# Performance work log

Hardware: AMD Instinct MI355X
Metric: run time of the kernel (lower is better)

## Reference

```python
import jax, jax.numpy as jnp
import numpy as np

DECAY = 0.6
THRESH = 0.6
MASK_T = 784 * 4  # default T in create_general_mask


def _make_mask(dim, c_min=10, c_max=50, min_dc=0.95, max_dc=0.99, T=MASK_T):
    # Faithful numpy port of create_general_mask (phase_shift_max=0.0 -> no shift).
    dcs = np.linspace(min_dc, max_dc, dim)
    cycles = np.linspace(c_min, c_max, dim)
    rows = []
    for cyc, dc in zip(cycles, dcs):
        cyc = int(np.ceil(cyc))
        on = int(np.ceil(dc * cyc))
        pat = [1] * on + [0] * (cyc - on)
        full = pat * (T // cyc) + pat[: T % cyc]
        rows.append(full)
    return jnp.asarray(np.array(rows, dtype=np.float32))  # [dim, T]


def setup_inputs() -> dict:
    key = jax.random.key(0)
    k1, k2, k3, k4, k5 = jax.random.split(key, 5)
    T, B, NTOKEN, NINP, H1, H2 = 128, 32, 32000, 256, 512, 512
    raw_input = jax.random.randint(k1, (T, B), 0, NTOKEN)
    enc_w = jax.random.uniform(k2, (NTOKEN, NINP), jnp.float32, -0.1, 0.1)
    # kaiming_uniform-like init: bound = sqrt(6 / fan_in), torch fan_in = dim 1
    b1 = float(np.sqrt(6.0 / H1))
    b2 = float(np.sqrt(6.0 / H2))
    fc1 = jax.random.uniform(k3, (NINP, H1), jnp.float32, -b1, b1)
    fc2 = jax.random.uniform(k4, (H1, H2), jnp.float32, -b2, b2)
    dec_w = jax.random.uniform(k5, (NTOKEN, H2), jnp.float32, -0.1, 0.1)
    dec_b = jnp.zeros((NTOKEN,), jnp.float32)
    mask1 = _make_mask(H1)
    mask2 = _make_mask(H2)
    return {"raw_input": raw_input, "enc_w": enc_w, "fc1": fc1, "fc2": fc2,
            "dec_w": dec_w, "dec_b": dec_b, "mask1": mask1, "mask2": mask2}


def _act(x):
    # ActFun.forward: heaviside spike
    return (x > 0.0).astype(x.dtype)


def reference(raw_input, enc_w, fc1, fc2, dec_w, dec_b, mask1, mask2):
    T, B = raw_input.shape
    emb = enc_w[raw_input]                    # [T, B, ninp] (dropout p=0 -> identity)
    m1 = mask1[:, :T].T                       # [T, H1]
    m2 = mask2[:, :T].T                       # [T, H2]

    def rhythm_update(fc, x, mem, m):
        state = x @ fc                        # [B, H]
        reset = (mem > THRESH).astype(x.dtype)
        new_mem = mem * (1.0 - reset) * DECAY + state
        mem = jnp.where(m == 0.0, mem, new_mem)   # mask broadcasts [H] -> [B, H]
        spike = _act(mem - THRESH) * m
        return mem, spike

    h1 = jnp.zeros((B, fc1.shape[1]), emb.dtype)
    h2 = jnp.zeros((B, fc2.shape[1]), emb.dtype)

    def step(carry, xs):
        h1m, h2m = carry
        x, ma, mb = xs
        h1m, s1 = rhythm_update(fc1, x, h1m, ma)
        h2m, s2 = rhythm_update(fc2, s1, h2m, mb)
        return (h1m, h2m), s2

    _, spikes = jax.lax.scan(step, (h1, h2), (emb, m1, m2))  # [T, B, H2]
    decoded = spikes @ dec_w.T + dec_b        # [T, B, ntoken]
    return decoded
```

## Files before the change

### kernel.cpp

```cpp
#include <hip/hip_runtime.h>


typedef __attribute__((ext_vector_type(8))) short short8;
typedef __attribute__((ext_vector_type(4))) float f32x4;
typedef __attribute__((ext_vector_type(8))) unsigned short us8;

__device__ __forceinline__ unsigned short f2bf(float f) {
    unsigned int u = __float_as_uint(f);
    unsigned int r = (u + 0x7FFFu + ((u >> 16) & 1u)) >> 16;
    return (unsigned short)r;
}

__global__ __launch_bounds__(256) void split_kernel(
    const float* __restrict__ w, unsigned short* __restrict__ w2, int n4)
{
    int i = blockIdx.x * 256 + threadIdx.x;
    if (i >= n4) return;
    float4 v = ((const float4*)w)[i];
    float vv[4] = {v.x, v.y, v.z, v.w};
    us8 o;
    #pragma unroll
    for (int c = 0; c < 4; ++c) {
        unsigned short hb = f2bf(vv[c]);
        float hf = __uint_as_float(((unsigned int)hb) << 16);
        o[2 * c]     = hb;
        o[2 * c + 1] = f2bf(vv[c] - hf);
    }
    ((us8*)w2)[i] = o;
}

__global__ __launch_bounds__(256) void gemm_f32_kernel(
    const float* __restrict__ A, const float* __restrict__ B,
    float* __restrict__ C, int M, int N, int K,
    const int* __restrict__ gidx, const float* __restrict__ gtable)
{
    __shared__ float As[16][64];
    __shared__ float Bs[16][64];
    int tid = threadIdx.x;
    int bn0 = blockIdx.x * 64, bm0 = blockIdx.y * 64;

    int lrowA = tid >> 2;
    int lkA   = (tid & 3) * 4;
    int lkB   = tid >> 4;
    int lnB   = (tid & 15) * 4;
    int ty = tid >> 4, tx = tid & 15;

    const float* Abase;
    size_t aoff;
    int grow = bm0 + lrowA;
    if (gidx) { Abase = gtable; aoff = (size_t)gidx[grow] * K; }
    else      { Abase = A;      aoff = (size_t)grow * K; }

    float acc[4][4];
    #pragma unroll
    for (int i = 0; i < 4; ++i)
        #pragma unroll
        for (int j = 0; j < 4; ++j) acc[i][j] = 0.f;

    for (int k0 = 0; k0 < K; k0 += 16) {
        float4 av = *(const float4*)(Abase + aoff + k0 + lkA);
        As[lkA + 0][lrowA] = av.x;
        As[lkA + 1][lrowA] = av.y;
        As[lkA + 2][lrowA] = av.z;
        As[lkA + 3][lrowA] = av.w;
        float4 bv = *(const float4*)(B + (size_t)(k0 + lkB) * N + bn0 + lnB);
        *(float4*)&Bs[lkB][lnB] = bv;
        __syncthreads();
        #pragma unroll
        for (int kk = 0; kk < 16; ++kk) {
            float4 aq = *(float4*)&As[kk][ty * 4];
            float4 bq = *(float4*)&Bs[kk][tx * 4];
            float aa[4] = {aq.x, aq.y, aq.z, aq.w};
            float bb[4] = {bq.x, bq.y, bq.z, bq.w};
            #pragma unroll
            for (int i = 0; i < 4; ++i)
                #pragma unroll
                for (int j = 0; j < 4; ++j) acc[i][j] += aa[i] * bb[j];
        }
        __syncthreads();
    }
    #pragma unroll
    for (int i = 0; i < 4; ++i) {
        float4 v = {acc[i][0], acc[i][1], acc[i][2], acc[i][3]};
        *(float4*)(C + (size_t)(bm0 + ty * 4 + i) * N + bn0 + tx * 4) = v;
    }
}

template <int DUP>
__global__ __launch_bounds__(64) void scan_kernel(
    const float* __restrict__ state, const float* __restrict__ mask,
    float* __restrict__ outF, unsigned int* __restrict__ outU)
{
    int tid = blockIdx.x * 64 + threadIdx.x;
    int b = tid >> 9, h = tid & 511;
    const float* mrow = mask + (size_t)h * 3136;
    float mem = 0.f;
    #pragma unroll
    for (int t = 0; t < 128; ++t) {
        size_t ridx = (size_t)(t * 32 + b) * 512 + h;
        float st = state[ridx];
        float m  = mrow[t];
        float nm = (mem > 0.6f) ? st : mem * 0.6f + st;
        mem = (m == 0.0f) ? mem : nm;
        float spf = (mem > 0.6f) ? m : 0.0f;
        if (DUP) {
            unsigned int bb = f2bf(spf);
            outU[ridx] = bb * 0x10001u;
        } else {
            outF[ridx] = spf;
        }
    }
}

__global__ __launch_bounds__(256) void gemm3_kernel(
    const unsigned short* __restrict__ A,
    const unsigned short* __restrict__ W,
    const float* __restrict__ bias, float* __restrict__ C)
{
    constexpr int K = 1024, NTOK = 32000;
    __shared__ unsigned short sA[128 * 64];
    __shared__ unsigned short sB[128 * 64];

    int tid  = threadIdx.x;
    int lane = tid & 63;
    int wid  = __builtin_amdgcn_readfirstlane(tid >> 6);

    int bid = blockIdx.x;
    int swz = (bid & 7) * 1000 + (bid >> 3);
    int mt = swz & 31;
    int nt = swz >> 5;
    int m0 = mt * 128, n0 = nt * 128;

    int wm = wid >> 1, wn = wid & 1;

    f32x4 acc[4][4];
    #pragma unroll
    for (int i = 0; i < 4; ++i)
        #pragma unroll
        for (int j = 0; j < 4; ++j) acc[i][j] = (f32x4){0.f, 0.f, 0.f, 0.f};

    for (int it = 0; it < 16; ++it) {
        int k0 = it * 64;

        #pragma unroll
        for (int i = 0; i < 4; ++i) {
            int q   = i * 256 + wid * 64 + lane;
            int row = q >> 3;
            int cb  = q & 7;
            int scb = cb ^ (row & 7);
            const unsigned short* ga = A + (size_t)(m0 + row) * K + k0 + scb * 8;
            const unsigned short* gb = W + (size_t)(n0 + row) * K + k0 + scb * 8;
            unsigned short* la = sA + (size_t)(i * 256 + wid * 64) * 8;
            unsigned short* lb = sB + (size_t)(i * 256 + wid * 64) * 8;
            __builtin_amdgcn_global_load_lds(
                (const __attribute__((address_space(1))) unsigned int*)ga,
                (__attribute__((address_space(3))) unsigned int*)la, 16, 0, 0);
            __builtin_amdgcn_global_load_lds(
                (const __attribute__((address_space(1))) unsigned int*)gb,
                (__attribute__((address_space(3))) unsigned int*)lb, 16, 0, 0);
        }
        __syncthreads();

        #pragma unroll
        for (int ks = 0; ks < 2; ++ks) {
            short8 fa[4], fb[4];
            int kb = ks * 64 + ((lane >> 4) << 4);
            #pragma unroll
            for (int f = 0; f < 4; ++f) {
                int rowA = wm * 64 + f * 16 + (lane & 15);
                int adA  = rowA * 128 + (kb ^ ((rowA & 7) << 4));
                fa[f] = *(const short8*)((const char*)sA + adA);
                int rowB = wn * 64 + f * 16 + (lane & 15);
                int adB  = rowB * 128 + (kb ^ ((rowB & 7) << 4));
                fb[f] = *(const short8*)((const char*)sB + adB);
            }
            #pragma unroll
            for (int mf = 0; mf < 4; ++mf)
                #pragma unroll
                for (int nf = 0; nf < 4; ++nf)
                    acc[mf][nf] = __builtin_amdgcn_mfma_f32_16x16x32_bf16(
                        fa[mf], fb[nf], acc[mf][nf], 0, 0, 0);
        }
        __syncthreads();
    }

    int lr = lane >> 4, lc = lane & 15;
    #pragma unroll
    for (int mf = 0; mf < 4; ++mf) {
        #pragma unroll
        for (int nf = 0; nf < 4; ++nf) {
            int gr = m0 + wm * 64 + mf * 16 + lr * 4;
            int gc = n0 + wn * 64 + nf * 16 + lc;
            float bv = bias[gc];
            f32x4 v = acc[mf][nf];
            #pragma unroll
            for (int j = 0; j < 4; ++j)
                C[(size_t)(gr + j) * NTOK + gc] = v[j] + bv;
        }
    }
}

extern "C" void kernel_launch(void* const* d_in, const int* in_sizes, int n_in,
                              void* d_out, int out_size, void* d_ws, size_t ws_size,
                              hipStream_t stream)
{
    const int*   raw   = (const int*)  d_in[0];
    const float* enc_w = (const float*)d_in[1];
    const float* fc1   = (const float*)d_in[2];
    const float* fc2   = (const float*)d_in[3];
    const float* dec_w = (const float*)d_in[4];
    const float* dec_b = (const float*)d_in[5];
    const float* mask1 = (const float*)d_in[6];
    const float* mask2 = (const float*)d_in[7];
    float* out = (float*)d_out;

    const int T = 128, B = 32, H1 = 512, H2 = 512, NINP = 256, NTOK = 32000;
    const int M = T * B;

    char* ws = (char*)d_ws;
    float*          st  = (float*)ws;
    float*          spF = (float*)(ws + (size_t)(8u << 20));
    unsigned int*   a2u = (unsigned int*)(ws + (size_t)(8u << 20));
    unsigned short* A2  = (unsigned short*)(ws + (size_t)(8u << 20));
    unsigned short* W2  = (unsigned short*)(ws + (size_t)(16u << 20));

    int n4 = NTOK * H2 / 4;
    split_kernel<<<(n4 + 255) / 256, 256, 0, stream>>>(dec_w, W2, n4);

    gemm_f32_kernel<<<dim3(H1 / 64, M / 64), 256, 0, stream>>>(
        nullptr, fc1, st, M, H1, NINP, raw, enc_w);

    scan_kernel<0><<<(B * H1) / 64, 64, 0, stream>>>(st, mask1, spF, nullptr);

    gemm_f32_kernel<<<dim3(H2 / 64, M / 64), 256, 0, stream>>>(
        spF, fc2, st, M, H2, H1, nullptr, nullptr);

    scan_kernel<1><<<(B * H2) / 64, 64, 0, stream>>>(st, mask2, nullptr, a2u);

    gemm3_kernel<<<(M / 128) * (NTOK / 128), 256, 0, stream>>>(A2, W2, dec_b, out);

    (void)in_sizes; (void)n_in; (void)out_size; (void)ws_size;
}
```

Before: 931.0 us.

## Rewrite decoder GEMM as 256x256 tile with 4-stage async LDS pipeline

```diff
diff --git a/kernel.cpp b/kernel.cpp
--- a/kernel.cpp
+++ b/kernel.cpp
@@ -4,11 +4,23 @@
 typedef __attribute__((ext_vector_type(8))) short short8;
 typedef __attribute__((ext_vector_type(4))) float f32x4;
 typedef __attribute__((ext_vector_type(8))) unsigned short us8;
+
+#define WAITVM(N) asm volatile("s_waitcnt vmcnt(" #N ")" ::: "memory")
 
 __device__ __forceinline__ unsigned short f2bf(float f) {
     unsigned int u = __float_as_uint(f);
     unsigned int r = (u + 0x7FFFu + ((u >> 16) & 1u)) >> 16;
     return (unsigned short)r;
+}
+
+__global__ __launch_bounds__(256) void maskT_kernel(
+    const float* __restrict__ m1, const float* __restrict__ m2,
+    float* __restrict__ t1, float* __restrict__ t2)
+{
+    int i = blockIdx.x * 256 + threadIdx.x;
+    int h = i >> 7, t = i & 127;
+    t1[t * 512 + h] = m1[(size_t)h * 3136 + t];
+    t2[t * 512 + h] = m2[(size_t)h * 3136 + t];
 }
 
 __global__ __launch_bounds__(256) void split_kernel(
@@ -88,110 +100,138 @@
 
 template <int DUP>
 __global__ __launch_bounds__(64) void scan_kernel(
-    const float* __restrict__ state, const float* __restrict__ mask,
+    const float* __restrict__ state, const float* __restrict__ maskT,
     float* __restrict__ outF, unsigned int* __restrict__ outU)
 {
     int tid = blockIdx.x * 64 + threadIdx.x;
     int b = tid >> 9, h = tid & 511;
-    const float* mrow = mask + (size_t)h * 3136;
     float mem = 0.f;
-    #pragma unroll
+    #pragma unroll 8
     for (int t = 0; t < 128; ++t) {
         size_t ridx = (size_t)(t * 32 + b) * 512 + h;
         float st = state[ridx];
-        float m  = mrow[t];
+        float m  = maskT[t * 512 + h];
         float nm = (mem > 0.6f) ? st : mem * 0.6f + st;
         mem = (m == 0.0f) ? mem : nm;
         float spf = (mem > 0.6f) ? m : 0.0f;
-        if (DUP) {
-            unsigned int bb = f2bf(spf);
-            outU[ridx] = bb * 0x10001u;
-        } else {
-            outF[ridx] = spf;
-        }
-    }
-}
-
-__global__ __launch_bounds__(256) void gemm3_kernel(
+        if (DUP) outU[ridx] = f2bf(spf) * 0x10001u;
+        else     outF[ridx] = spf;
+    }
+}
+
+__global__ __launch_bounds__(512, 2) void gemm3_kernel(
     const unsigned short* __restrict__ A,
     const unsigned short* __restrict__ W,
     const float* __restrict__ bias, float* __restrict__ C)
 {
     constexpr int K = 1024, NTOK = 32000;
-    __shared__ unsigned short sA[128 * 64];
-    __shared__ unsigned short sB[128 * 64];
+    __shared__ char lds[131072];
 
     int tid  = threadIdx.x;
     int lane = tid & 63;
     int wid  = __builtin_amdgcn_readfirstlane(tid >> 6);
 
     int bid = blockIdx.x;
-    int swz = (bid & 7) * 1000 + (bid >> 3);
-    int mt = swz & 31;
-    int nt = swz >> 5;
-    int m0 = mt * 128, n0 = nt * 128;
-
-    int wm = wid >> 1, wn = wid & 1;
-
-    f32x4 acc[4][4];
-    #pragma unroll
-    for (int i = 0; i < 4; ++i)
+    int swz = (bid & 7) * 250 + (bid >> 3);
+    int mt = swz & 15;
+    int nt = swz >> 4;
+    int m0 = mt * 256, n0 = nt * 256;
+
+    int wm = wid >> 2, wn = wid & 3;
+
+    const unsigned short* srcB[4];
+    int dstOff[4];
+    #pragma unroll
+    for (int i = 0; i < 4; ++i) {
+        int q   = i * 512 + tid;
+        int isB = q >> 10;
+        int qq  = q & 1023;
+        int row = qq >> 2;
+        int cp  = qq & 3;
+        int c   = cp ^ ((row + (row >> 2)) & 3);
+        srcB[i] = (isB ? W + (size_t)(n0 + row) * K
+                       : A + (size_t)(m0 + row) * K) + c * 8;
+        dstOff[i] = (i * 512 + wid * 64) * 16;
+    }
+
+    int r = lane & 15, co = lane >> 4;
+    int aOff[8], bOff[4];
+    #pragma unroll
+    for (int mf = 0; mf < 8; ++mf) {
+        int row = wm * 128 + mf * 16 + r;
+        aOff[mf] = row * 64 + ((co ^ ((row + (row >> 2)) & 3)) * 16);
+    }
+    #pragma unroll
+    for (int nf = 0; nf < 4; ++nf) {
+        int row = wn * 64 + nf * 16 + r;
+        bOff[nf] = 16384 + row * 64 + ((co ^ ((row + (row >> 2)) & 3)) * 16);
+    }
+
+    f32x4 acc[8][4];
+    #pragma unroll
+    for (int i = 0; i < 8; ++i)
         #pragma unroll
         for (int j = 0; j < 4; ++j) acc[i][j] = (f32x4){0.f, 0.f, 0.f, 0.f};
 
-    for (int it = 0; it < 16; ++it) {
-        int k0 = it * 64;
-
+    auto STAGE = [&](int slot, int kt) {
         #pragma unroll
         for (int i = 0; i < 4; ++i) {
-            int q   = i * 256 + wid * 64 + lane;
-            int row = q >> 3;
-            int cb  = q & 7;
-            int scb = cb ^ (row & 7);
-            const unsigned short* ga = A + (size_t)(m0 + row) * K + k0 + scb * 8;
-            const unsigned short* gb = W + (size_t)(n0 + row) * K + k0 + scb * 8;
-            unsigned short* la = sA + (size_t)(i * 256 + wid * 64) * 8;
-            unsigned short* lb = sB + (size_t)(i * 256 + wid * 64) * 8;
             __builtin_amdgcn_global_load_lds(
-                (const __attribute__((address_space(1))) unsigned int*)ga,
-                (__attribute__((address_space(3))) unsigned int*)la, 16, 0, 0);
-            __builtin_amdgcn_global_load_lds(
-                (const __attribute__((address_space(1))) unsigned int*)gb,
-                (__attribute__((address_space(3))) unsigned int*)lb, 16, 0, 0);
+                (const __attribute__((address_space(1))) unsigned int*)(srcB[i] + kt * 32),
+                (__attribute__((address_space(3))) unsigned int*)(lds + (slot << 15) + dstOff[i]),
+                16, 0, 0);
         }
-        __syncthreads();
-
-        #pragma unroll
-        for (int ks = 0; ks < 2; ++ks) {
-            short8 fa[4], fb[4];
-            int kb = ks * 64 + ((lane >> 4) << 4);
+    };
+    auto COMPUTE = [&](int t) {
+        const char* base = lds + ((t & 3) << 15);
+        short8 fa[8], fb[4];
+        #pragma unroll
+        for (int mf = 0; mf < 8; ++mf) fa[mf] = *(const short8*)(base + aOff[mf]);
+        #pragma unroll
+        for (int nf = 0; nf < 4; ++nf) fb[nf] = *(const short8*)(base + bOff[nf]);
+        __builtin_amdgcn_s_setprio(1);
+        #pragma unroll
+        for (int mf = 0; mf < 8; ++mf)
             #pragma unroll
-            for (int f = 0; f < 4; ++f) {
-                int rowA = wm * 64 + f * 16 + (lane & 15);
-                int adA  = rowA * 128 + (kb ^ ((rowA & 7) << 4));
-                fa[f] = *(const short8*)((const char*)sA + adA);
-                int rowB = wn * 64 + f * 16 + (lane & 15);
-                int adB  = rowB * 128 + (kb ^ ((rowB & 7) << 4));
-                fb[f] = *(const short8*)((const char*)sB + adB);
-            }
-            #pragma unroll
-            for (int mf = 0; mf < 4; ++mf)
-                #pragma unroll
-                for (int nf = 0; nf < 4; ++nf)
-                    acc[mf][nf] = __builtin_amdgcn_mfma_f32_16x16x32_bf16(
-                        fa[mf], fb[nf], acc[mf][nf], 0, 0, 0);
-        }
-        __syncthreads();
-    }
+            for (int nf = 0; nf < 4; ++nf)
+                acc[mf][nf] = __builtin_amdgcn_mfma_f32_16x16x32_bf16(
+                    fa[mf], fb[nf], acc[mf][nf], 0, 0, 0);
+        __builtin_amdgcn_s_setprio(0);
+    };
+
+    STAGE(0, 0);
+    STAGE(1, 1);
+    STAGE(2, 2);
+    WAITVM(8);
+    __builtin_amdgcn_s_barrier();
+    __builtin_amdgcn_sched_barrier(0);
+
+    #pragma unroll 4
+    for (int t = 0; t < 29; ++t) {
+        STAGE((t + 3) & 3, t + 3);
+        COMPUTE(t);
+        WAITVM(8);
+        __builtin_amdgcn_s_barrier();
+        __builtin_amdgcn_sched_barrier(0);
+    }
+    COMPUTE(29);
+    WAITVM(4);
+    __builtin_amdgcn_s_barrier();
+    __builtin_amdgcn_sched_barrier(0);
+    COMPUTE(30);
+    WAITVM(0);
+    __builtin_amdgcn_s_barrier();
+    __builtin_amdgcn_sched_barrier(0);
+    COMPUTE(31);
 
     int lr = lane >> 4, lc = lane & 15;
     #pragma unroll
-    for (int mf = 0; mf < 4; ++mf) {
-        #pragma unroll
-        for (int nf = 0; nf < 4; ++nf) {
-            int gr = m0 + wm * 64 + mf * 16 + lr * 4;
-            int gc = n0 + wn * 64 + nf * 16 + lc;
-            float bv = bias[gc];
+    for (int nf = 0; nf < 4; ++nf) {
+        int gc = n0 + wn * 64 + nf * 16 + lc;
+        float bv = bias[gc];
+        #pragma unroll
+        for (int mf = 0; mf < 8; ++mf) {
+            int gr = m0 + wm * 128 + mf * 16 + lr * 4;
             f32x4 v = acc[mf][nf];
             #pragma unroll
             for (int j = 0; j < 4; ++j)
@@ -214,8 +254,8 @@
     const float* mask2 = (const float*)d_in[7];
     float* out = (float*)d_out;
 
-    const int T = 128, B = 32, H1 = 512, H2 = 512, NINP = 256, NTOK = 32000;
-    const int M = T * B;
+    const int H1 = 512, H2 = 512, NINP = 256, NTOK = 32000;
+    const int M = 128 * 32;
 
     char* ws = (char*)d_ws;
     float*          st  = (float*)ws;
@@ -223,6 +263,10 @@
     unsigned int*   a2u = (unsigned int*)(ws + (size_t)(8u << 20));
     unsigned short* A2  = (unsigned short*)(ws + (size_t)(8u << 20));
     unsigned short* W2  = (unsigned short*)(ws + (size_t)(16u << 20));
+    float* mT1 = (float*)d_out;
+    float* mT2 = (float*)d_out + 65536;
+
+    maskT_kernel<<<256, 256, 0, stream>>>(mask1, mask2, mT1, mT2);
 
     int n4 = NTOK * H2 / 4;
     split_kernel<<<(n4 + 255) / 256, 256, 0, stream>>>(dec_w, W2, n4);
@@ -230,14 +274,14 @@
     gemm_f32_kernel<<<dim3(H1 / 64, M / 64), 256, 0, stream>>>(
         nullptr, fc1, st, M, H1, NINP, raw, enc_w);
 
-    scan_kernel<0><<<(B * H1) / 64, 64, 0, stream>>>(st, mask1, spF, nullptr);
+    scan_kernel<0><<<256, 64, 0, stream>>>(st, mT1, spF, nullptr);
 
     gemm_f32_kernel<<<dim3(H2 / 64, M / 64), 256, 0, stream>>>(
         spF, fc2, st, M, H2, H1, nullptr, nullptr);
 
-    scan_kernel<1><<<(B * H2) / 64, 64, 0, stream>>>(st, mask2, nullptr, a2u);
-
-    gemm3_kernel<<<(M / 128) * (NTOK / 128), 256, 0, stream>>>(A2, W2, dec_b, out);
+    scan_kernel<1><<<256, 64, 0, stream>>>(st, mT2, nullptr, a2u);
+
+    gemm3_kernel<<<(M / 256) * (NTOK / 256), 512, 0, stream>>>(A2, W2, dec_b, out);
 
     (void)in_sizes; (void)n_in; (void)out_size; (void)ws_size;
 }
```

Result: slower. 964.2 us (+3.6%).
